# Kernel optimization log

Measured on AMD Instinct MI355X. Metric: run time of the kernel, lower is better.

Reference implementation:

```python
import jax, jax.numpy as jnp
import numpy as np

RES_UP_RATIO = 0.05   # reserve_up_ratio (mgr.args default)
RES_DN_RATIO = 0.02   # reserve_dn_ratio
REQ_UP_RATIO = 0.02   # system_reserve_up_ratio
REQ_DN_RATIO = 0.02   # system_reserve_dn_ratio


def _build_K(G):
    """Static constraint matrix of the per-timestep LP over x=[P, R_up, R_dn] (n=3G).
    Row 0 is the equality sum(P)=D; remaining rows are <= inequalities."""
    n = 3 * G
    m = 1 + 4 * G + 2
    K = np.zeros((m, n), dtype=np.float32)
    I = np.eye(G, dtype=np.float32)
    K[0, :G] = 1.0                      # sum_g P = D
    r = 1
    K[r:r+G, :G] = I;  K[r:r+G, G:2*G] = I;  r += G      # P + R_up <= pmax
    K[r:r+G, :G] = -I; K[r:r+G, 2*G:3*G] = I; r += G     # -P + R_dn <= -pmin
    K[r:r+G, :G] = I;  r += G                             # P <= pmax
    K[r:r+G, :G] = -I; r += G                             # -P <= -pmin
    K[r, G:2*G] = -1.0; r += 1                            # -sum R_up <= -req_up*D
    K[r, 2*G:3*G] = -1.0                                  # -sum R_dn <= -req_dn*D
    return K


def _solve_da_lp(forecast, pmin, pmax, b, n_iters):
    """Batched PDHG (Chambolle-Pock) solve of all B*T per-timestep LPs.
    Returns P, R_up, R_dn with shape (B, T, G)."""
    B, T = forecast.shape
    G = b.shape[0]
    Knp = _build_K(G)
    L = float(np.linalg.norm(Knp, 2))          # static spectral norm of K
    tau = sigma = 0.9 / L
    K = jnp.asarray(Knp)
    m, n = K.shape
    # objective coefficients over x=[P, R_up, R_dn] (Cost = b*P + c is affine)
    c_obj = jnp.concatenate([b, RES_UP_RATIO * b, RES_DN_RATIO * b])  # (n,)
    # rhs q: (B, T, m)
    q = jnp.concatenate([
        forecast[..., None],
        jnp.broadcast_to(pmax, (B, T, G)),
        jnp.broadcast_to(-pmin, (B, T, G)),
        jnp.broadcast_to(pmax, (B, T, G)),
        jnp.broadcast_to(-pmin, (B, T, G)),
        -REQ_UP_RATIO * forecast[..., None],
        -REQ_DN_RATIO * forecast[..., None],
    ], axis=-1)
    ineq = (jnp.arange(m) > 0)  # row 0 = equality dual (unprojected)

    x0 = jnp.zeros((B, T, n), dtype=forecast.dtype)
    y0 = jnp.zeros((B, T, m), dtype=forecast.dtype)

    def step(carry, _):
        x, y = carry
        x_new = jnp.maximum(x - tau * (c_obj + jnp.einsum('btm,mn->btn', y, K)), 0.0)
        x_bar = 2.0 * x_new - x
        y_new = y + sigma * (jnp.einsum('btn,mn->btm', x_bar, K) - q)
        y_new = jnp.where(ineq, jnp.maximum(y_new, 0.0), y_new)
        return (x_new, y_new), None

    (x, _), _ = jax.lax.scan(step, (x0, y0), None, length=n_iters)
    P = x[..., :G]
    Ru = x[..., G:2*G]
    Rd = x[..., 2*G:3*G]
    return P, Ru, Rd


def setup_inputs() -> dict:
    key = jax.random.key(0)
    k1, k2, k3, k4 = jax.random.split(key, 4)
    G, B, T = 50, 128, 24
    pmax = 100.0 + 400.0 * jax.random.uniform(k1, (G,), dtype=jnp.float32)
    pmin = 0.1 * pmax
    b = 20.0 + 30.0 * jax.random.uniform(k2, (G,), dtype=jnp.float32)
    c = 100.0 * jax.random.uniform(k3, (G,), dtype=jnp.float32)
    lo, hi = jnp.sum(pmin), jnp.sum(pmax)
    # feasible demand: comfortably inside [sum pmin, sum pmax] so reserves exist
    forecast = lo + (0.35 + 0.3 * jax.random.uniform(k4, (B, T), dtype=jnp.float32)) * (hi - lo)
    return {"forecast": forecast, "pmin": pmin, "pmax": pmax, "b": b, "c": c, "n_iters": 300}


def reference(forecast, pmin, pmax, b, c, n_iters):
    P, Ru, Rd = _solve_da_lp(forecast, pmin, pmax, b, n_iters)  # (B,T,G)
    # match torch layout (B, G, T)
    P_DA = jnp.swapaxes(P, 1, 2)
    R_up = jnp.swapaxes(Ru, 1, 2)
    R_dn = jnp.swapaxes(Rd, 1, 2)
    Cost_DA = b[None, :, None] * P_DA + c[None, :, None]
    ru_price = (RES_UP_RATIO * b)[None, :, None]
    rd_price = (RES_DN_RATIO * b)[None, :, None]
    obj = Cost_DA.sum((1, 2)) + (ru_price * R_up).sum((1, 2)) + (rd_price * R_dn).sum((1, 2))
    return (P_DA, R_up, R_dn, obj, Cost_DA)
```

## Files before the change

kernel.cpp:

```cpp
#include <hip/hip_runtime.h>
#include <math.h>

#define G   50
#define T   24
#define B   128
#define NLP (B * T)
#define SZ  (B * G * T)

typedef float v2f __attribute__((ext_vector_type(2)));


__device__ __forceinline__ v2f vmax0(v2f v) {
    v2f z = {0.f, 0.f};
    return __builtin_elementwise_max(v, z);
}

template <int CTRL>
__device__ __forceinline__ float dpp_mov(float x) {
    int r = __builtin_amdgcn_update_dpp(0, __float_as_int(x), CTRL, 0xf, 0xf, true);
    return __int_as_float(r);
}

__device__ __forceinline__ void row_sum3(float& a, float& b, float& c) {
    asm("s_nop 1\n\t"
        "v_add_f32_dpp %0, %0, %0 row_ror:1 row_mask:0xf bank_mask:0xf\n\t"
        "v_add_f32_dpp %1, %1, %1 row_ror:1 row_mask:0xf bank_mask:0xf\n\t"
        "v_add_f32_dpp %2, %2, %2 row_ror:1 row_mask:0xf bank_mask:0xf\n\t"
        "v_add_f32_dpp %0, %0, %0 row_ror:2 row_mask:0xf bank_mask:0xf\n\t"
        "v_add_f32_dpp %1, %1, %1 row_ror:2 row_mask:0xf bank_mask:0xf\n\t"
        "v_add_f32_dpp %2, %2, %2 row_ror:2 row_mask:0xf bank_mask:0xf\n\t"
        "v_add_f32_dpp %0, %0, %0 row_ror:4 row_mask:0xf bank_mask:0xf\n\t"
        "v_add_f32_dpp %1, %1, %1 row_ror:4 row_mask:0xf bank_mask:0xf\n\t"
        "v_add_f32_dpp %2, %2, %2 row_ror:4 row_mask:0xf bank_mask:0xf\n\t"
        "v_add_f32_dpp %0, %0, %0 row_ror:8 row_mask:0xf bank_mask:0xf\n\t"
        "v_add_f32_dpp %1, %1, %1 row_ror:8 row_mask:0xf bank_mask:0xf\n\t"
        "v_add_f32_dpp %2, %2, %2 row_ror:8 row_mask:0xf bank_mask:0xf"
        : "+v"(a), "+v"(b), "+v"(c));
}

__device__ __forceinline__ float row_sum1(float a) {
    a += dpp_mov<0x121>(a);
    a += dpp_mov<0x122>(a);
    a += dpp_mov<0x124>(a);
    a += dpp_mov<0x128>(a);
    return a;
}

__global__ __launch_bounds__(64)
void pdhg_lp_kernel(const float* __restrict__ forecast,
                    const float* __restrict__ pmin,
                    const float* __restrict__ pmax,
                    const float* __restrict__ bcost,
                    const float* __restrict__ ccost,
                    const int*   __restrict__ n_iters_p,
                    float* __restrict__ out,
                    float* __restrict__ ws_partial,
                    float tau)
{
    const int lane = threadIdx.x;
    const int lh   = lane & 15;
    const int row  = lane >> 4;
    const int lp   = blockIdx.x * 4 + row;
    const int b    = lp / T;
    const int t    = lp - b * T;
    const int n_iters = n_iters_p[0];

    const int  gA0 = lh,      gA1 = lh + 16;
    const int  gB0 = lh + 32;
    const int  gB1 = lh + 48;
    const bool vB1 = (lh < 2);

    v2f bjA  = { bcost[gA0], bcost[gA1] };
    v2f bjB  = { bcost[gB0], vB1 ? bcost[gB1] : 0.f };
    v2f cjA  = { ccost[gA0], ccost[gA1] };
    v2f cjB  = { ccost[gB0], vB1 ? ccost[gB1] : 0.f };
    v2f pmxA = { pmax[gA0],  pmax[gA1] };
    v2f pmxB = { pmax[gB0],  vB1 ? pmax[gB1] : 0.f };
    v2f pmnA = { pmin[gA0],  pmin[gA1] };
    v2f pmnB = { pmin[gB0],  vB1 ? pmin[gB1] : 0.f };
    const float f = forecast[lp];

    const float ts  = tau * tau;
    const float BIG = 1e30f;

    v2f tcPA  = tau * bjA;
    v2f tcPB  = tau * bjB;           if (!vB1) tcPB.y  = BIG;
    v2f tcRuA = (tau * 0.05f) * bjA;
    v2f tcRuB = (tau * 0.05f) * bjB; if (!vB1) tcRuB.y = BIG;
    v2f tcRdA = (tau * 0.02f) * bjA;
    v2f tcRdB = (tau * 0.02f) * bjB; if (!vB1) tcRdB.y = BIG;
    v2f tspmxA = ts * pmxA, tspmxB = ts * pmxB;
    v2f tspmnA = ts * pmnA, tspmnB = ts * pmnB;
    const float tsf   = ts * f;
    const float tsreq = ts * 0.02f * f;

    v2f PA = {0,0}, PB = {0,0}, RuA = {0,0}, RuB = {0,0}, RdA = {0,0}, RdB = {0,0};
    v2f z1A = {0,0}, z1B = {0,0}, z2A = {0,0}, z2B = {0,0};
    v2f z3A = {0,0}, z3B = {0,0}, z4A = {0,0}, z4B = {0,0};
    float z0 = 0.f, zru = 0.f, zrd = 0.f;

    for (int it = 0; it < n_iters; ++it) {
        v2f z0v = { z0, z0 };
        v2f zruv = { zru, zru };
        v2f zrdv = { zrd, zrd };
        v2f gPA = (z1A - z2A) + (z3A - z4A) + z0v;
        v2f gPB = (z1B - z2B) + (z3B - z4B) + z0v;
        v2f PnA = vmax0(PA - tcPA - gPA);
        v2f PnB = vmax0(PB - tcPB - gPB);
        v2f RunA = vmax0(RuA - tcRuA - z1A + zruv);
        v2f RunB = vmax0(RuB - tcRuB - z1B + zruv);
        v2f RdnA = vmax0(RdA - tcRdA - z2A + zrdv);
        v2f RdnB = vmax0(RdB - tcRdB - z2B + zrdv);

        v2f PbA  = 2.f * PnA  - PA,  PbB  = 2.f * PnB  - PB;
        v2f RubA = 2.f * RunA - RuA, RubB = 2.f * RunB - RuB;
        v2f RdbA = 2.f * RdnA - RdA, RdbB = 2.f * RdnB - RdB;
        PA = PnA; PB = PnB; RuA = RunA; RuB = RunB; RdA = RdnA; RdB = RdnB;

        v2f tP = PbA + PbB, tRu = RubA + RubB, tRd = RdbA + RdbB;
        float sP  = tP.x  + tP.y;
        float sRu = tRu.x + tRu.y;
        float sRd = tRd.x + tRd.y;
        row_sum3(sP, sRu, sRd);

        z0  = z0 + ts * sP - tsf;
        z1A = vmax0(z1A + ts * (PbA + RubA) - tspmxA);
        z1B = vmax0(z1B + ts * (PbB + RubB) - tspmxB);
        z2A = vmax0(z2A + ts * (RdbA - PbA) + tspmnA);
        z2B = vmax0(z2B + ts * (RdbB - PbB) + tspmnB);
        z3A = vmax0(z3A + ts * PbA - tspmxA);
        z3B = vmax0(z3B + ts * PbB - tspmxB);
        z4A = vmax0(z4A - ts * PbA + tspmnA);
        z4B = vmax0(z4B - ts * PbB + tspmnB);
        zru = fmaxf(zru + tsreq - ts * sRu, 0.f);
        zrd = fmaxf(zrd + tsreq - ts * sRd, 0.f);
    }

    const v2f costA = bjA * PA + cjA;
    const v2f costB = bjB * PB + cjB;
    {
        const int bgt = b * (G * T) + t;
        const int a0 = bgt + gA0 * T, a1 = bgt + gA1 * T, b0 = bgt + gB0 * T;
        out[a0] = PA.x;  out[SZ + a0] = RuA.x;  out[2*SZ + a0] = RdA.x;  out[3*SZ + B + a0] = costA.x;
        out[a1] = PA.y;  out[SZ + a1] = RuA.y;  out[2*SZ + a1] = RdA.y;  out[3*SZ + B + a1] = costA.y;
        out[b0] = PB.x;  out[SZ + b0] = RuB.x;  out[2*SZ + b0] = RdB.x;  out[3*SZ + B + b0] = costB.x;
        if (vB1) {
            const int b1 = bgt + gB1 * T;
            out[b1] = PB.y;  out[SZ + b1] = RuB.y;  out[2*SZ + b1] = RdB.y;  out[3*SZ + B + b1] = costB.y;
        }
    }

    if (ws_partial) {
        v2f lo = costA + (0.05f * bjA) * RuA + (0.02f * bjA) * RdA
               + costB + (0.05f * bjB) * RuB + (0.02f * bjB) * RdB;
        float tot = row_sum1(lo.x + lo.y);
        if (lh == 0) ws_partial[lp] = tot;
    }
}

__global__ __launch_bounds__(64)
void obj_final_kernel(const float* __restrict__ ws_partial, float* __restrict__ out)
{
    const int b = blockIdx.x * 64 + threadIdx.x;
    if (b < B) {
        float s = 0.f;
        #pragma unroll
        for (int t = 0; t < T; ++t) s += ws_partial[b * T + t];
        out[3 * SZ + b] = s;
    }
}

__global__ __launch_bounds__(256)
void obj_kernel(const float* __restrict__ bcost, float* __restrict__ out)
{
    const int b = blockIdx.x;
    const float* Ru = out + SZ     + (size_t)b * (G * T);
    const float* Rd = out + 2 * SZ + (size_t)b * (G * T);
    const float* C  = out + 3 * SZ + B + (size_t)b * (G * T);

    float s = 0.f;
    for (int i = threadIdx.x; i < G * T; i += 256) {
        const int g = i / T;
        const float bg = bcost[g];
        s += C[i] + 0.05f * bg * Ru[i] + 0.02f * bg * Rd[i];
    }
    __shared__ float sm[16];
    s = row_sum1(s);
    if ((threadIdx.x & 15) == 0) sm[threadIdx.x >> 4] = s;
    __syncthreads();
    if (threadIdx.x == 0) {
        float tot = 0.f;
        #pragma unroll
        for (int i = 0; i < 16; ++i) tot += sm[i];
        out[3 * SZ + b] = tot;
    }
}

extern "C" void kernel_launch(void* const* d_in, const int* in_sizes, int n_in,
                              void* d_out, int out_size, void* d_ws, size_t ws_size,
                              hipStream_t stream) {
    const float* forecast = (const float*)d_in[0];
    const float* pmin_p   = (const float*)d_in[1];
    const float* pmax_p   = (const float*)d_in[2];
    const float* b_p      = (const float*)d_in[3];
    const float* c_p      = (const float*)d_in[4];
    const int*   niter_p  = (const int*)  d_in[5];
    float* out = (float*)d_out;

    const double L = sqrt((105.0 + sqrt(17.0)) * 0.5);
    const float tau = (float)(0.9 / L);

    const bool use_ws = (ws_size >= (size_t)NLP * sizeof(float));
    float* wsp = use_ws ? (float*)d_ws : nullptr;

    pdhg_lp_kernel<<<NLP / 4, 64, 0, stream>>>(forecast, pmin_p, pmax_p,
                                               b_p, c_p, niter_p, out, wsp, tau);
    if (use_ws) {
        obj_final_kernel<<<(B + 63) / 64, 64, 0, stream>>>(wsp, out);
    } else {
        obj_kernel<<<B, 256, 0, stream>>>(b_p, out);
    }
}
```

Before: 136.0 us.

## Map each LP to 32 lanes instead of 16, halving per-lane generator work

Each LP now spans half a wavefront (32 lanes), and each lane holds 2 generators instead of 4, so per-iteration VALU work per lane drops by half. The grid doubles to 1536 waves. Cross-row sums use DPP within 16-lane rows plus a ds_swizzle to combine the two rows, and the swizzle latency is overlapped with the z1..z4 updates. The cost is twice as many waves and an added LDS-path swizzle with a waitcnt on the serial iteration chain.

After: 147.2 us. 8.2% more time.

```diff
diff --git a/kernel.cpp b/kernel.cpp
--- a/kernel.cpp
+++ b/kernel.cpp
@@ -46,6 +46,15 @@
     return a;
 }
 
+__device__ __forceinline__ float half_sum1(float a) {
+    a = row_sum1(a);
+    float t;
+    asm("ds_swizzle_b32 %0, %1 offset:0x401f\n\t"
+        "s_waitcnt lgkmcnt(0)"
+        : "=&v"(t) : "v"(a));
+    return a + t;
+}
+
 __global__ __launch_bounds__(64)
 void pdhg_lp_kernel(const float* __restrict__ forecast,
                     const float* __restrict__ pmin,
@@ -58,103 +67,91 @@
                     float tau)
 {
     const int lane = threadIdx.x;
-    const int lh   = lane & 15;
-    const int row  = lane >> 4;
-    const int lp   = blockIdx.x * 4 + row;
+    const int l    = lane & 31;
+    const int half = lane >> 5;
+    const int lp   = blockIdx.x * 2 + half;
     const int b    = lp / T;
     const int t    = lp - b * T;
     const int n_iters = n_iters_p[0];
 
-    const int  gA0 = lh,      gA1 = lh + 16;
-    const int  gB0 = lh + 32;
-    const int  gB1 = lh + 48;
-    const bool vB1 = (lh < 2);
-
-    v2f bjA  = { bcost[gA0], bcost[gA1] };
-    v2f bjB  = { bcost[gB0], vB1 ? bcost[gB1] : 0.f };
-    v2f cjA  = { ccost[gA0], ccost[gA1] };
-    v2f cjB  = { ccost[gB0], vB1 ? ccost[gB1] : 0.f };
-    v2f pmxA = { pmax[gA0],  pmax[gA1] };
-    v2f pmxB = { pmax[gB0],  vB1 ? pmax[gB1] : 0.f };
-    v2f pmnA = { pmin[gA0],  pmin[gA1] };
-    v2f pmnB = { pmin[gB0],  vB1 ? pmin[gB1] : 0.f };
+    const int  g0 = l;
+    const int  g1 = l + 32;
+    const bool v1 = (l < 18);
+
+    v2f bj  = { bcost[g0], v1 ? bcost[g1] : 0.f };
+    v2f cj  = { ccost[g0], v1 ? ccost[g1] : 0.f };
+    v2f pmx = { pmax[g0],  v1 ? pmax[g1]  : 0.f };
+    v2f pmn = { pmin[g0],  v1 ? pmin[g1]  : 0.f };
     const float f = forecast[lp];
 
     const float ts  = tau * tau;
     const float BIG = 1e30f;
 
-    v2f tcPA  = tau * bjA;
-    v2f tcPB  = tau * bjB;           if (!vB1) tcPB.y  = BIG;
-    v2f tcRuA = (tau * 0.05f) * bjA;
-    v2f tcRuB = (tau * 0.05f) * bjB; if (!vB1) tcRuB.y = BIG;
-    v2f tcRdA = (tau * 0.02f) * bjA;
-    v2f tcRdB = (tau * 0.02f) * bjB; if (!vB1) tcRdB.y = BIG;
-    v2f tspmxA = ts * pmxA, tspmxB = ts * pmxB;
-    v2f tspmnA = ts * pmnA, tspmnB = ts * pmnB;
+    v2f tcP  = tau * bj;           if (!v1) tcP.y  = BIG;
+    v2f tcRu = (tau * 0.05f) * bj; if (!v1) tcRu.y = BIG;
+    v2f tcRd = (tau * 0.02f) * bj; if (!v1) tcRd.y = BIG;
+    v2f tspmx = ts * pmx, tspmn = ts * pmn;
     const float tsf   = ts * f;
     const float tsreq = ts * 0.02f * f;
 
-    v2f PA = {0,0}, PB = {0,0}, RuA = {0,0}, RuB = {0,0}, RdA = {0,0}, RdB = {0,0};
-    v2f z1A = {0,0}, z1B = {0,0}, z2A = {0,0}, z2B = {0,0};
-    v2f z3A = {0,0}, z3B = {0,0}, z4A = {0,0}, z4B = {0,0};
+    v2f P = {0,0}, Ru = {0,0}, Rd = {0,0};
+    v2f z1 = {0,0}, z2 = {0,0}, z3 = {0,0}, z4 = {0,0};
     float z0 = 0.f, zru = 0.f, zrd = 0.f;
 
     for (int it = 0; it < n_iters; ++it) {
-        v2f z0v = { z0, z0 };
+        v2f z0v  = { z0,  z0  };
         v2f zruv = { zru, zru };
         v2f zrdv = { zrd, zrd };
-        v2f gPA = (z1A - z2A) + (z3A - z4A) + z0v;
-        v2f gPB = (z1B - z2B) + (z3B - z4B) + z0v;
-        v2f PnA = vmax0(PA - tcPA - gPA);
-        v2f PnB = vmax0(PB - tcPB - gPB);
-        v2f RunA = vmax0(RuA - tcRuA - z1A + zruv);
-        v2f RunB = vmax0(RuB - tcRuB - z1B + zruv);
-        v2f RdnA = vmax0(RdA - tcRdA - z2A + zrdv);
-        v2f RdnB = vmax0(RdB - tcRdB - z2B + zrdv);
-
-        v2f PbA  = 2.f * PnA  - PA,  PbB  = 2.f * PnB  - PB;
-        v2f RubA = 2.f * RunA - RuA, RubB = 2.f * RunB - RuB;
-        v2f RdbA = 2.f * RdnA - RdA, RdbB = 2.f * RdnB - RdB;
-        PA = PnA; PB = PnB; RuA = RunA; RuB = RunB; RdA = RdnA; RdB = RdnB;
-
-        v2f tP = PbA + PbB, tRu = RubA + RubB, tRd = RdbA + RdbB;
-        float sP  = tP.x  + tP.y;
-        float sRu = tRu.x + tRu.y;
-        float sRd = tRd.x + tRd.y;
+        v2f gP  = (z1 - z2) + (z3 - z4) + z0v;
+        v2f Pn  = vmax0(P  - tcP  - gP);
+        v2f Run = vmax0(Ru - tcRu - z1 + zruv);
+        v2f Rdn = vmax0(Rd - tcRd - z2 + zrdv);
+
+        v2f Pb  = 2.f * Pn  - P;
+        v2f Rub = 2.f * Run - Ru;
+        v2f Rdb = 2.f * Rdn - Rd;
+        P = Pn; Ru = Run; Rd = Rdn;
+
+        float sP  = Pb.x  + Pb.y;
+        float sRu = Rub.x + Rub.y;
+        float sRd = Rdb.x + Rdb.y;
         row_sum3(sP, sRu, sRd);
 
+        float xP, xRu, xRd;
+        asm("ds_swizzle_b32 %0, %3 offset:0x401f\n\t"
+            "ds_swizzle_b32 %1, %4 offset:0x401f\n\t"
+            "ds_swizzle_b32 %2, %5 offset:0x401f"
+            : "=&v"(xP), "=&v"(xRu), "=&v"(xRd)
+            : "v"(sP), "v"(sRu), "v"(sRd));
+
+        z1 = vmax0(z1 + ts * (Pb + Rub) - tspmx);
+        z2 = vmax0(z2 + ts * (Rdb - Pb) + tspmn);
+        z3 = vmax0(z3 + ts * Pb - tspmx);
+        z4 = vmax0(z4 - ts * Pb + tspmn);
+
+        asm("s_waitcnt lgkmcnt(0)" : "+v"(xP), "+v"(xRu), "+v"(xRd));
+        sP += xP; sRu += xRu; sRd += xRd;
+
         z0  = z0 + ts * sP - tsf;
-        z1A = vmax0(z1A + ts * (PbA + RubA) - tspmxA);
-        z1B = vmax0(z1B + ts * (PbB + RubB) - tspmxB);
-        z2A = vmax0(z2A + ts * (RdbA - PbA) + tspmnA);
-        z2B = vmax0(z2B + ts * (RdbB - PbB) + tspmnB);
-        z3A = vmax0(z3A + ts * PbA - tspmxA);
-        z3B = vmax0(z3B + ts * PbB - tspmxB);
-        z4A = vmax0(z4A - ts * PbA + tspmnA);
-        z4B = vmax0(z4B - ts * PbB + tspmnB);
         zru = fmaxf(zru + tsreq - ts * sRu, 0.f);
         zrd = fmaxf(zrd + tsreq - ts * sRd, 0.f);
     }
 
-    const v2f costA = bjA * PA + cjA;
-    const v2f costB = bjB * PB + cjB;
+    const v2f cost = bj * P + cj;
     {
         const int bgt = b * (G * T) + t;
-        const int a0 = bgt + gA0 * T, a1 = bgt + gA1 * T, b0 = bgt + gB0 * T;
-        out[a0] = PA.x;  out[SZ + a0] = RuA.x;  out[2*SZ + a0] = RdA.x;  out[3*SZ + B + a0] = costA.x;
-        out[a1] = PA.y;  out[SZ + a1] = RuA.y;  out[2*SZ + a1] = RdA.y;  out[3*SZ + B + a1] = costA.y;
-        out[b0] = PB.x;  out[SZ + b0] = RuB.x;  out[2*SZ + b0] = RdB.x;  out[3*SZ + B + b0] = costB.x;
-        if (vB1) {
-            const int b1 = bgt + gB1 * T;
-            out[b1] = PB.y;  out[SZ + b1] = RuB.y;  out[2*SZ + b1] = RdB.y;  out[3*SZ + B + b1] = costB.y;
+        const int a0 = bgt + g0 * T;
+        out[a0] = P.x;  out[SZ + a0] = Ru.x;  out[2*SZ + a0] = Rd.x;  out[3*SZ + B + a0] = cost.x;
+        if (v1) {
+            const int a1 = bgt + g1 * T;
+            out[a1] = P.y;  out[SZ + a1] = Ru.y;  out[2*SZ + a1] = Rd.y;  out[3*SZ + B + a1] = cost.y;
         }
     }
 
     if (ws_partial) {
-        v2f lo = costA + (0.05f * bjA) * RuA + (0.02f * bjA) * RdA
-               + costB + (0.05f * bjB) * RuB + (0.02f * bjB) * RdB;
-        float tot = row_sum1(lo.x + lo.y);
-        if (lh == 0) ws_partial[lp] = tot;
+        v2f lo = cost + (0.05f * bj) * Ru + (0.02f * bj) * Rd;
+        float tot = half_sum1(lo.x + lo.y);
+        if (l == 0) ws_partial[lp] = tot;
     }
 }
 
@@ -213,7 +210,7 @@
     const bool use_ws = (ws_size >= (size_t)NLP * sizeof(float));
     float* wsp = use_ws ? (float*)d_ws : nullptr;
 
-    pdhg_lp_kernel<<<NLP / 4, 64, 0, stream>>>(forecast, pmin_p, pmax_p,
+    pdhg_lp_kernel<<<NLP / 2, 64, 0, stream>>>(forecast, pmin_p, pmax_p,
                                                b_p, c_p, niter_p, out, wsp, tau);
     if (use_ws) {
         obj_final_kernel<<<(B + 63) / 64, 64, 0, stream>>>(wsp, out);
```
